# Kernel optimization log

Measured on AMD Instinct MI355X. Metric: run time of the kernel, lower is better.

The kernel has to match this reference:

```python
import jax, jax.numpy as jnp
import numpy as np

N_ITER = 10
EPS = 1e-20
REG = 1e-6


def _nmf(Tn, Vn, Yn):
    # Tn [I,K], Vn [K,J], Yn [I,J] complex. T,V are strictly positive, so
    # torch's .abs() on Rn is the identity.
    Rn = Tn @ Vn
    Y_d_R = jnp.abs(Yn) ** 2 / (Rn ** 2 + EPS)
    Rn_d = 1.0 / (Rn + EPS)
    Tn = Tn * jnp.sqrt((Y_d_R @ Vn.T) / (Rn_d @ Vn.T + EPS))
    Vn = Vn * jnp.sqrt((Tn.T @ Y_d_R) / (Tn.T @ Rn_d + EPS))
    Rn_new = Tn @ Vn
    return Tn, Vn, Rn_new


def _forward(X, T0, V0):
    M, J, I, _ = X.shape
    N = M
    # [M,J,I,2] real -> [I,M,J] complex64
    X_c = (X[..., 0] + 1j * X[..., 1]).astype(jnp.complex64).transpose(2, 0, 1)
    eye = jnp.eye(M, dtype=jnp.complex64)
    W = jnp.broadcast_to(eye[None], (I, M, M)).astype(jnp.complex64) + jnp.zeros((I, M, M), jnp.complex64)
    Y = jnp.einsum('inm,imj->inj', W, X_c)  # [I,N,J]
    T = T0
    V = V0

    def body(carry, _):
        W, Y, T, V = carry
        for n in range(N):  # N == 2, structurally small static loop
            Tn, Vn, Rn = _nmf(T[:, :, n], V[:, :, n], Y[:, n, :])
            T = T.at[:, :, n].set(Tn)
            V = V.at[:, :, n].set(Vn)
            inv_sqrt_Rn = jnp.sqrt(1.0 / (Rn + EPS))  # [I,J] real
            Xw = X_c * inv_sqrt_Rn[:, None, :]  # [I,M,J] complex
            D = Xw @ jnp.conj(Xw).transpose(0, 2, 1) / J + REG * eye[None]  # [I,M,M]
            A = W @ D
            e_n = jnp.broadcast_to(eye[:, n][None, :, None], (D.shape[0], M, 1))
            b = jnp.linalg.solve(A, e_n)  # [I,M,1]
            bH = jnp.conj(b).transpose(0, 2, 1)
            denom = jnp.sqrt((bH @ D @ b).real + EPS)  # [I,1,1]
            w = jnp.conj((b / denom)[:, :, 0])  # [I,M]
            W = W.at[:, n, :].set(w)
        Y = jnp.einsum('inm,imj->inj', W, X_c)
        return (W, Y, T, V), None

    (W, Y, T, V), _ = jax.lax.scan(body, (W, Y, T, V), None, length=N_ITER)
    Y_out = Y.transpose(1, 2, 0)  # [N,J,I]
    return jnp.stack([Y_out.real, Y_out.imag], axis=-1)  # [N,J,I,2]


def setup_inputs() -> dict:
    key = jax.random.key(0)
    k1, k2, k3 = jax.random.split(key, 3)
    M, J, I, K = 2, 1024, 1025, 8
    X = jax.random.normal(k1, (M, J, I, 2), dtype=jnp.float32)
    T0 = jax.random.uniform(k2, (I, K, M), dtype=jnp.float32) * (1 - 1e-8) + 1e-8
    V0 = jax.random.uniform(k3, (K, J, M), dtype=jnp.float32) * (1 - 1e-8) + 1e-8
    return {"X": X, "T0": T0, "V0": V0}


def reference(X, T0, V0):
    return _forward(X, T0, V0)
```

## Files before the change

### kernel.cpp

```cpp
#include <hip/hip_runtime.h>
#include <math.h>

#define I_DIM 1025
#define J_DIM 1024
#define K_DIM 8
#define N_ITER 10
#define EPS 1e-20f
#define REG 1e-6f
#define MODE_CD  1
#define MODE_NMF 2

__device__ __forceinline__ float __frcp(float x){ return __builtin_amdgcn_rcpf(x); }

__device__ __forceinline__ float2 cmul(float2 a, float2 b){
  return make_float2(a.x*b.x - a.y*b.y, a.x*b.y + a.y*b.x);
}
__device__ __forceinline__ float2 cadd(float2 a, float2 b){
  return make_float2(a.x+b.x, a.y+b.y);
}
__device__ __forceinline__ float2 csub(float2 a, float2 b){
  return make_float2(a.x-b.x, a.y-b.y);
}
__device__ __forceinline__ float2 cconj(float2 a){ return make_float2(a.x, -a.y); }
__device__ __forceinline__ float2 cscale(float2 a, float s){ return make_float2(a.x*s, a.y*s); }
__device__ __forceinline__ float2 cdivc(float2 a, float2 d){
  float inv = 1.0f/(d.x*d.x + d.y*d.y);
  return make_float2((a.x*d.x + a.y*d.y)*inv, (a.y*d.x - a.x*d.y)*inv);
}

__global__ void k_init(const float* __restrict__ T0, const float* __restrict__ V0,
                       float* __restrict__ Tw, float* __restrict__ Vw, float2* __restrict__ Wm){
  int tid = blockIdx.x*blockDim.x + threadIdx.x;
  if (tid < 2*K_DIM*I_DIM){
    int i = tid % I_DIM; int rest = tid / I_DIM;
    int k = rest & 7, n = rest >> 3;
    Tw[tid] = T0[(i*K_DIM+k)*2 + n];
  }
  if (tid < 2*K_DIM*J_DIM){
    int n = tid/(K_DIM*J_DIM), rem = tid%(K_DIM*J_DIM);
    int k = rem/J_DIM, j = rem%J_DIM;
    Vw[tid] = V0[(k*J_DIM+j)*2 + n];
  }
  if (tid < I_DIM*4){
    int rc = tid & 3;
    Wm[tid] = make_float2((rc==0||rc==3)?1.0f:0.0f, 0.0f);
  }
}

__global__ void k_txpose(const float2* __restrict__ Xin, float4* __restrict__ Xc4){
  __shared__ float4 tile[32][33];
  int i0 = blockIdx.x*32, j0 = blockIdx.y*32;
  int tx = threadIdx.x, ty = threadIdx.y;
  #pragma unroll
  for (int r=0;r<4;r++){
    int jl = ty + r*8; int i = i0 + tx;
    if (i < I_DIM){
      float2 a = Xin[(size_t)(0*J_DIM + j0 + jl)*I_DIM + i];
      float2 b = Xin[(size_t)(1*J_DIM + j0 + jl)*I_DIM + i];
      tile[jl][tx] = make_float4(a.x, a.y, b.x, b.y);
    }
  }
  __syncthreads();
  #pragma unroll
  for (int r=0;r<4;r++){
    int il = ty + r*8; int i = i0 + il;
    if (i < I_DIM) Xc4[(size_t)i*J_DIM + j0 + tx] = tile[tx][il];
  }
}

__global__ __launch_bounds__(256) void k_cda(const float4* __restrict__ Xc4,
      float* __restrict__ Tw, float* __restrict__ Told, const float* __restrict__ Vw,
      float2* __restrict__ Wm, int mode){
  int i = blockIdx.x, tid = threadIdx.x;
  int n = tid >> 7, jl = tid & 127;
  __shared__ float redD[4][4];
  __shared__ float redT[4][16];
  __shared__ float wsh[8];

  float t[8];
  #pragma unroll
  for (int k=0;k<8;k++) t[k] = Tw[(size_t)(n*K_DIM+k)*I_DIM + i];

  const float* vb = Vw + (size_t)(n*K_DIM)*J_DIM + jl;
  float r_s[8] = {0,0,0,0,0,0,0,0};
  #pragma unroll
  for (int k=0;k<8;k++){
    #pragma unroll
    for (int s=0;s<8;s++) r_s[s] += t[k]*vb[k*J_DIM + 128*s];
  }
  float q_s[8];
  #pragma unroll
  for (int s=0;s<8;s++) q_s[s] = __frcp(r_s[s] + EPS);

  const float4* xb = Xc4 + (size_t)i*J_DIM + jl;
  float4 x_s[8];
  #pragma unroll
  for (int s=0;s<8;s++) x_s[s] = xb[128*s];

  if (mode & MODE_CD){
    float d00=0.0f, d11=0.0f, dre=0.0f, dim_=0.0f;
    #pragma unroll
    for (int s=0;s<8;s++){
      float4 x = x_s[s]; float q = q_s[s];
      d00 += (x.x*x.x + x.y*x.y)*q;
      d11 += (x.z*x.z + x.w*x.w)*q;
      dre += (x.x*x.z + x.y*x.w)*q;
      dim_ += (x.y*x.z - x.x*x.w)*q;
    }
    #pragma unroll
    for (int off=32; off>0; off>>=1){
      d00 += __shfl_down(d00,off); d11 += __shfl_down(d11,off);
      dre += __shfl_down(dre,off); dim_ += __shfl_down(dim_,off);
    }
    {
      int lane = tid&63, wv = tid>>6;
      if (lane==0){ redD[wv][0]=d00; redD[wv][1]=d11; redD[wv][2]=dre; redD[wv][3]=dim_; }
    }
    __syncthreads();
    if (tid==0){
      const float invJ = 1.0f/(float)J_DIM;
      float D[2][4];
      #pragma unroll
      for (int c=0;c<4;c++){
        D[0][c] = (redD[0][c]+redD[1][c])*invJ;
        D[1][c] = (redD[2][c]+redD[3][c])*invJ;
      }
      float2 w00 = Wm[i*4+0], w01 = Wm[i*4+1], w10 = Wm[i*4+2], w11 = Wm[i*4+3];
      #pragma unroll
      for (int nn=0;nn<2;nn++){
        float d00_ = D[nn][0] + REG, d11_ = D[nn][1] + REG;
        float2 d01 = make_float2(D[nn][2], D[nn][3]);
        float2 d10 = cconj(d01);
        float2 A00 = cadd(cscale(w00, d00_), cmul(w01, d10));
        float2 A01 = cadd(cmul(w00, d01), cscale(w01, d11_));
        float2 A10 = cadd(cscale(w10, d00_), cmul(w11, d10));
        float2 A11 = cadd(cmul(w10, d01), cscale(w11, d11_));
        float2 det = csub(cmul(A00,A11), cmul(A01,A10));
        float2 bu0, bu1;
        if (nn==0){ bu0 = A11; bu1 = make_float2(-A10.x, -A10.y); }
        else      { bu0 = make_float2(-A01.x, -A01.y); bu1 = A00; }
        float2 b0 = cdivc(bu0, det);
        float2 b1 = cdivc(bu1, det);
        float quad = d00_*(b0.x*b0.x + b0.y*b0.y) + d11_*(b1.x*b1.x + b1.y*b1.y);
        float2 u = cmul(d01, b1);
        quad += 2.0f*(b0.x*u.x + b0.y*u.y);
        float inv = 1.0f/sqrtf(quad + EPS);
        float2 wn0 = make_float2(b0.x*inv, -b0.y*inv);
        float2 wn1 = make_float2(b1.x*inv, -b1.y*inv);
        if (nn==0){ w00=wn0; w01=wn1; } else { w10=wn0; w11=wn1; }
      }
      Wm[i*4+0]=w00; Wm[i*4+1]=w01; Wm[i*4+2]=w10; Wm[i*4+3]=w11;
      wsh[0]=w00.x; wsh[1]=w00.y; wsh[2]=w01.x; wsh[3]=w01.y;
      wsh[4]=w10.x; wsh[5]=w10.y; wsh[6]=w11.x; wsh[7]=w11.y;
    }
  } else {
    if (tid < 4){ float2 w = Wm[i*4+tid]; wsh[tid*2]=w.x; wsh[tid*2+1]=w.y; }
  }
  __syncthreads();
  if (!(mode & MODE_NMF)) return;

  if ((tid & 127) < 8){
    int kk = tid & 7;
    Told[(size_t)(n*K_DIM+kk)*I_DIM + i] = t[kk];
  }

  float2 w0 = make_float2(wsh[n*4+0], wsh[n*4+1]);
  float2 w1 = make_float2(wsh[n*4+2], wsh[n*4+3]);
  float p_s[8];
  #pragma unroll
  for (int s=0;s<8;s++){
    float4 x = x_s[s];
    float yre = w0.x*x.x - w0.y*x.y + w1.x*x.z - w1.y*x.w;
    float yim = w0.x*x.y + w0.y*x.x + w1.x*x.w + w1.y*x.z;
    float q = q_s[s];
    p_s[s] = (yre*yre + yim*yim)*q*q;
  }
  float aN[8], aD[8];
  #pragma unroll
  for (int k=0;k<8;k++){
    float sn = 0.0f, sd = 0.0f;
    #pragma unroll
    for (int s=0;s<8;s++){
      float v = vb[k*J_DIM + 128*s];
      sn += p_s[s]*v; sd += q_s[s]*v;
    }
    aN[k] = sn; aD[k] = sd;
  }
  #pragma unroll
  for (int k=0;k<8;k++){
    #pragma unroll
    for (int off=32; off>0; off>>=1){
      aN[k] += __shfl_down(aN[k],off);
      aD[k] += __shfl_down(aD[k],off);
    }
  }
  {
    int lane = tid&63, wv = tid>>6;
    if (lane==0){
      #pragma unroll
      for (int k=0;k<8;k++){ redT[wv][k]=aN[k]; redT[wv][k+8]=aD[k]; }
    }
  }
  __syncthreads();
  if ((tid & 127) < 8){
    int kk = tid & 7;
    int wb = (tid>>7)*2;
    float ns = redT[wb][kk]   + redT[wb+1][kk];
    float ds = redT[wb][kk+8] + redT[wb+1][kk+8];
    size_t ti = (size_t)(n*K_DIM+kk)*I_DIM + i;
    Tw[ti] = Tw[ti]*sqrtf(ns*__frcp(ds + EPS));
  }
}

__global__ __launch_bounds__(256) void k_vupd(const float4* __restrict__ Xc4,
      const float* __restrict__ Tw, const float* __restrict__ Told,
      float* __restrict__ Vw, const float2* __restrict__ Wm){
  int n = blockIdx.y;
  int tid = threadIdx.x;
  int jj = tid & 3, ii = tid >> 2;
  int j = blockIdx.x*4 + jj;
  float v[8];
  #pragma unroll
  for (int k=0;k<8;k++) v[k] = Vw[(size_t)(n*K_DIM+k)*J_DIM + j];
  float aN[8] = {0,0,0,0,0,0,0,0};
  float aD[8] = {0,0,0,0,0,0,0,0};
  const float* tob = Told + (size_t)(n*K_DIM)*I_DIM;
  const float* tnb = Tw   + (size_t)(n*K_DIM)*I_DIM;
  #pragma unroll 2
  for (int i=ii; i<I_DIM; i+=64){
    float to[8], tn[8];
    #pragma unroll
    for (int k=0;k<8;k++){ to[k] = tob[k*I_DIM + i]; tn[k] = tnb[k*I_DIM + i]; }
    float4 wv = *(const float4*)&Wm[i*4 + n*2];
    float4 x  = Xc4[(size_t)i*J_DIM + j];
    float r = to[0]*v[0]+to[1]*v[1]+to[2]*v[2]+to[3]*v[3]
            + to[4]*v[4]+to[5]*v[5]+to[6]*v[6]+to[7]*v[7];
    float yre = wv.x*x.x - wv.y*x.y + wv.z*x.z - wv.w*x.w;
    float yim = wv.x*x.y + wv.y*x.x + wv.z*x.w + wv.w*x.z;
    float q = __frcp(r + EPS);
    float p = (yre*yre + yim*yim)*q*q;
    #pragma unroll
    for (int k=0;k<8;k++){ aN[k] += tn[k]*p; aD[k] += tn[k]*q; }
  }
  #pragma unroll
  for (int k=0;k<8;k++){
    #pragma unroll
    for (int off=32; off>=4; off>>=1){
      aN[k] += __shfl_down(aN[k],off);
      aD[k] += __shfl_down(aD[k],off);
    }
  }
  __shared__ float red[4][4][16];
  int wv_ = tid>>6, lane = tid&63;
  if (lane < 4){
    #pragma unroll
    for (int k=0;k<8;k++){ red[wv_][lane][k]=aN[k]; red[wv_][lane][k+8]=aD[k]; }
  }
  __syncthreads();
  if (tid < 32){
    int jj2 = tid>>3, k = tid&7;
    float num = red[0][jj2][k]+red[1][jj2][k]+red[2][jj2][k]+red[3][jj2][k];
    float den = red[0][jj2][k+8]+red[1][jj2][k+8]+red[2][jj2][k+8]+red[3][jj2][k+8];
    size_t vi = (size_t)(n*K_DIM+k)*J_DIM + blockIdx.x*4 + jj2;
    Vw[vi] *= sqrtf(num*__frcp(den + EPS));
  }
}

__global__ void k_final(const float4* __restrict__ Xc4, const float2* __restrict__ Wm,
                        float2* __restrict__ out){
  __shared__ float2 yt[2][32][33];
  int i0 = blockIdx.x*32, j0 = blockIdx.y*32;
  int tx = threadIdx.x, ty = threadIdx.y;
  int j = j0 + tx;
  #pragma unroll
  for (int r=0;r<4;r++){
    int il = ty + r*8; int i = i0 + il;
    if (i < I_DIM){
      float4 x = Xc4[(size_t)i*J_DIM + j];
      #pragma unroll
      for (int n=0;n<2;n++){
        float2 a = Wm[i*4+n*2+0], b = Wm[i*4+n*2+1];
        float2 y;
        y.x = a.x*x.x - a.y*x.y + b.x*x.z - b.y*x.w;
        y.y = a.x*x.y + a.y*x.x + b.x*x.w + b.y*x.z;
        yt[n][tx][il] = y;
      }
    }
  }
  __syncthreads();
  int i = i0 + tx;
  if (i < I_DIM){
    #pragma unroll
    for (int n=0;n<2;n++){
      #pragma unroll
      for (int r=0;r<4;r++){
        int jl = ty + r*8;
        out[(size_t)(n*J_DIM + j0 + jl)*I_DIM + i] = yt[n][jl][tx];
      }
    }
  }
}

extern "C" void kernel_launch(void* const* d_in, const int* in_sizes, int n_in,
                              void* d_out, int out_size, void* d_ws, size_t ws_size,
                              hipStream_t stream){
  const float* X  = (const float*)d_in[0];
  const float* T0 = (const float*)d_in[1];
  const float* V0 = (const float*)d_in[2];

  char* ws = (char*)d_ws;
  size_t off = 0;
  auto alloc = [&](size_t bytes)->char*{
    char* p = ws + off; off += (bytes + 255) & ~(size_t)255; return p;
  };
  float4* Xc4  = (float4*)alloc((size_t)I_DIM*J_DIM*sizeof(float4));
  float*  Tw   = (float*) alloc((size_t)2*K_DIM*I_DIM*sizeof(float));
  float*  Told = (float*) alloc((size_t)2*K_DIM*I_DIM*sizeof(float));
  float*  Vw   = (float*) alloc((size_t)2*K_DIM*J_DIM*sizeof(float));
  float2* Wm   = (float2*)alloc((size_t)I_DIM*4*sizeof(float2));

  k_init<<<65, 256, 0, stream>>>(T0, V0, Tw, Vw, Wm);
  k_txpose<<<dim3(33,32), dim3(32,8), 0, stream>>>((const float2*)X, Xc4);
  k_cda<<<I_DIM, 256, 0, stream>>>(Xc4, Tw, Told, Vw, Wm, MODE_NMF);
  for (int it=0; it<N_ITER; it++){
    k_vupd<<<dim3(J_DIM/4, 2), 256, 0, stream>>>(Xc4, Tw, Told, Vw, Wm);
    int mode = (it < N_ITER-1) ? (MODE_CD|MODE_NMF) : MODE_CD;
    k_cda<<<I_DIM, 256, 0, stream>>>(Xc4, Tw, Told, Vw, Wm, mode);
  }
  k_final<<<dim3(33,32), dim3(32,8), 0, stream>>>(Xc4, Wm, (float2*)d_out);
}
```

Baseline: 311.7 us.

## Add j-major copy of X for V-update and fuse init with transpose

The setup kernel now merges the T/V/W initialisation with the X transpose and also writes a second, j-major copy of the packed complex input (XcT). The V-update kernel reads this copy, so consecutive i in a thread's loop touch contiguous memory. The CD/NMF kernel drops its register-cached x_s array and reloads X from memory in each phase, and both main kernels get a min-blocks launch bound of 4 to raise occupancy. The cost is a second 16 MB copy of X, extra reloads of X, and possible register pressure or spills under the tighter launch bounds.

```diff
diff --git a/kernel.cpp b/kernel.cpp
--- a/kernel.cpp
+++ b/kernel.cpp
@@ -28,36 +28,39 @@
   return make_float2((a.x*d.x + a.y*d.y)*inv, (a.y*d.x - a.x*d.y)*inv);
 }
 
-__global__ void k_init(const float* __restrict__ T0, const float* __restrict__ V0,
-                       float* __restrict__ Tw, float* __restrict__ Vw, float2* __restrict__ Wm){
-  int tid = blockIdx.x*blockDim.x + threadIdx.x;
-  if (tid < 2*K_DIM*I_DIM){
-    int i = tid % I_DIM; int rest = tid / I_DIM;
+__global__ __launch_bounds__(256) void k_setup(
+    const float2* __restrict__ X, const float* __restrict__ T0, const float* __restrict__ V0,
+    float4* __restrict__ Xc4, float4* __restrict__ XcT,
+    float* __restrict__ Tw, float* __restrict__ Vw, float2* __restrict__ Wm){
+  __shared__ float4 tile[32][33];
+  int b = blockIdx.x, tid = threadIdx.x;
+  int gtid = b*256 + tid;
+  if (gtid < 2*K_DIM*I_DIM){
+    int i = gtid % I_DIM; int rest = gtid / I_DIM;
     int k = rest & 7, n = rest >> 3;
-    Tw[tid] = T0[(i*K_DIM+k)*2 + n];
-  }
-  if (tid < 2*K_DIM*J_DIM){
-    int n = tid/(K_DIM*J_DIM), rem = tid%(K_DIM*J_DIM);
+    Tw[gtid] = T0[(i*K_DIM+k)*2 + n];
+  }
+  if (gtid < 2*K_DIM*J_DIM){
+    int n = gtid/(K_DIM*J_DIM), rem = gtid%(K_DIM*J_DIM);
     int k = rem/J_DIM, j = rem%J_DIM;
-    Vw[tid] = V0[(k*J_DIM+j)*2 + n];
-  }
-  if (tid < I_DIM*4){
-    int rc = tid & 3;
-    Wm[tid] = make_float2((rc==0||rc==3)?1.0f:0.0f, 0.0f);
-  }
-}
-
-__global__ void k_txpose(const float2* __restrict__ Xin, float4* __restrict__ Xc4){
-  __shared__ float4 tile[32][33];
-  int i0 = blockIdx.x*32, j0 = blockIdx.y*32;
-  int tx = threadIdx.x, ty = threadIdx.y;
+    Vw[gtid] = V0[(k*J_DIM+j)*2 + n];
+  }
+  if (gtid < I_DIM*4){
+    int rc = gtid & 3;
+    Wm[gtid] = make_float2((rc==0||rc==3)?1.0f:0.0f, 0.0f);
+  }
+  int ib = b / 32, jb = b % 32;
+  int i0 = ib*32, j0 = jb*32;
+  int tx = tid & 31, ty = tid >> 5;
   #pragma unroll
   for (int r=0;r<4;r++){
     int jl = ty + r*8; int i = i0 + tx;
     if (i < I_DIM){
-      float2 a = Xin[(size_t)(0*J_DIM + j0 + jl)*I_DIM + i];
-      float2 b = Xin[(size_t)(1*J_DIM + j0 + jl)*I_DIM + i];
-      tile[jl][tx] = make_float4(a.x, a.y, b.x, b.y);
+      float2 a = X[(size_t)(0*J_DIM + j0 + jl)*I_DIM + i];
+      float2 c = X[(size_t)(1*J_DIM + j0 + jl)*I_DIM + i];
+      float4 val = make_float4(a.x, a.y, c.x, c.y);
+      tile[jl][tx] = val;
+      XcT[(size_t)(j0+jl)*I_DIM + i] = val;
     }
   }
   __syncthreads();
@@ -68,7 +71,7 @@
   }
 }
 
-__global__ __launch_bounds__(256) void k_cda(const float4* __restrict__ Xc4,
+__global__ __launch_bounds__(256, 4) void k_cda(const float4* __restrict__ Xc4,
       float* __restrict__ Tw, float* __restrict__ Told, const float* __restrict__ Vw,
       float2* __restrict__ Wm, int mode){
   int i = blockIdx.x, tid = threadIdx.x;
@@ -93,15 +96,12 @@
   for (int s=0;s<8;s++) q_s[s] = __frcp(r_s[s] + EPS);
 
   const float4* xb = Xc4 + (size_t)i*J_DIM + jl;
-  float4 x_s[8];
-  #pragma unroll
-  for (int s=0;s<8;s++) x_s[s] = xb[128*s];
 
   if (mode & MODE_CD){
     float d00=0.0f, d11=0.0f, dre=0.0f, dim_=0.0f;
     #pragma unroll
     for (int s=0;s<8;s++){
-      float4 x = x_s[s]; float q = q_s[s];
+      float4 x = xb[128*s]; float q = q_s[s];
       d00 += (x.x*x.x + x.y*x.y)*q;
       d11 += (x.z*x.z + x.w*x.w)*q;
       dre += (x.x*x.z + x.y*x.w)*q;
@@ -169,7 +169,7 @@
   float p_s[8];
   #pragma unroll
   for (int s=0;s<8;s++){
-    float4 x = x_s[s];
+    float4 x = xb[128*s];
     float yre = w0.x*x.x - w0.y*x.y + w1.x*x.z - w1.y*x.w;
     float yim = w0.x*x.y + w0.y*x.x + w1.x*x.w + w1.y*x.z;
     float q = q_s[s];
@@ -212,7 +212,7 @@
   }
 }
 
-__global__ __launch_bounds__(256) void k_vupd(const float4* __restrict__ Xc4,
+__global__ __launch_bounds__(256, 4) void k_vupd(const float4* __restrict__ XcT,
       const float* __restrict__ Tw, const float* __restrict__ Told,
       float* __restrict__ Vw, const float2* __restrict__ Wm){
   int n = blockIdx.y;
@@ -226,13 +226,14 @@
   float aD[8] = {0,0,0,0,0,0,0,0};
   const float* tob = Told + (size_t)(n*K_DIM)*I_DIM;
   const float* tnb = Tw   + (size_t)(n*K_DIM)*I_DIM;
+  const float4* xcb = XcT + (size_t)j*I_DIM;
   #pragma unroll 2
   for (int i=ii; i<I_DIM; i+=64){
     float to[8], tn[8];
     #pragma unroll
     for (int k=0;k<8;k++){ to[k] = tob[k*I_DIM + i]; tn[k] = tnb[k*I_DIM + i]; }
     float4 wv = *(const float4*)&Wm[i*4 + n*2];
-    float4 x  = Xc4[(size_t)i*J_DIM + j];
+    float4 x  = xcb[i];
     float r = to[0]*v[0]+to[1]*v[1]+to[2]*v[2]+to[3]*v[3]
             + to[4]*v[4]+to[5]*v[5]+to[6]*v[6]+to[7]*v[7];
     float yre = wv.x*x.x - wv.y*x.y + wv.z*x.z - wv.w*x.w;
@@ -304,9 +305,9 @@
 extern "C" void kernel_launch(void* const* d_in, const int* in_sizes, int n_in,
                               void* d_out, int out_size, void* d_ws, size_t ws_size,
                               hipStream_t stream){
-  const float* X  = (const float*)d_in[0];
-  const float* T0 = (const float*)d_in[1];
-  const float* V0 = (const float*)d_in[2];
+  const float2* X  = (const float2*)d_in[0];
+  const float*  T0 = (const float*)d_in[1];
+  const float*  V0 = (const float*)d_in[2];
 
   char* ws = (char*)d_ws;
   size_t off = 0;
@@ -314,16 +315,16 @@
     char* p = ws + off; off += (bytes + 255) & ~(size_t)255; return p;
   };
   float4* Xc4  = (float4*)alloc((size_t)I_DIM*J_DIM*sizeof(float4));
+  float4* XcT  = (float4*)alloc((size_t)J_DIM*I_DIM*sizeof(float4));
   float*  Tw   = (float*) alloc((size_t)2*K_DIM*I_DIM*sizeof(float));
   float*  Told = (float*) alloc((size_t)2*K_DIM*I_DIM*sizeof(float));
   float*  Vw   = (float*) alloc((size_t)2*K_DIM*J_DIM*sizeof(float));
   float2* Wm   = (float2*)alloc((size_t)I_DIM*4*sizeof(float2));
 
-  k_init<<<65, 256, 0, stream>>>(T0, V0, Tw, Vw, Wm);
-  k_txpose<<<dim3(33,32), dim3(32,8), 0, stream>>>((const float2*)X, Xc4);
+  k_setup<<<33*32, 256, 0, stream>>>(X, T0, V0, Xc4, XcT, Tw, Vw, Wm);
   k_cda<<<I_DIM, 256, 0, stream>>>(Xc4, Tw, Told, Vw, Wm, MODE_NMF);
   for (int it=0; it<N_ITER; it++){
-    k_vupd<<<dim3(J_DIM/4, 2), 256, 0, stream>>>(Xc4, Tw, Told, Vw, Wm);
+    k_vupd<<<dim3(J_DIM/4, 2), 256, 0, stream>>>(XcT, Tw, Told, Vw, Wm);
     int mode = (it < N_ITER-1) ? (MODE_CD|MODE_NMF) : MODE_CD;
     k_cda<<<I_DIM, 256, 0, stream>>>(Xc4, Tw, Told, Vw, Wm, mode);
   }
```

After: 466.4 us. 49.6% more time.
